# Optimization experiments

Hardware: AMD Instinct MI355X
Metric: run time of the kernel (lower is better)

## Reference

```python
import jax, jax.numpy as jnp
import numpy as np

HEADS = 16


def _rope(t):
    # t: [B, H, S, hd]. lucidrains RotaryEmbedding(dim=hd//2): rotates first hd//2
    # channels with interleaved pairs, theta=10000; remaining channels pass through.
    hd = t.shape[-1]
    rot = hd // 2
    S = t.shape[-2]
    inv_freq = 1.0 / (10000.0 ** (jnp.arange(0, rot, 2, dtype=jnp.float32) / rot))  # [rot//2]
    ang = jnp.arange(S, dtype=jnp.float32)[:, None] * inv_freq[None, :]             # [S, rot//2]
    ang = jnp.repeat(ang, 2, axis=-1)                                               # [S, rot]
    cos, sin = jnp.cos(ang), jnp.sin(ang)
    tl, tr = t[..., :rot], t[..., rot:]
    p = tl.reshape(*tl.shape[:-1], rot // 2, 2)
    rh = jnp.stack([-p[..., 1], p[..., 0]], axis=-1).reshape(tl.shape)              # rotate_half
    tl = tl * cos + rh * sin
    return jnp.concatenate([tl, tr], axis=-1)


def setup_inputs() -> dict:
    key = jax.random.key(0)
    ks = jax.random.split(key, 3)
    D = 1024
    return {
        "x": jax.random.normal(ks[0], (2, 2048, D), dtype=jnp.float32),
        "w_qkv": jax.random.normal(ks[1], (D, 3 * D), dtype=jnp.float32) * 0.02,
        "b_qkv": jnp.zeros((3 * D,), dtype=jnp.float32),
        "w_out": jax.random.normal(ks[2], (D, D), dtype=jnp.float32) * 0.02,
        "b_out": jnp.zeros((D,), dtype=jnp.float32),
        "ln_gamma": jnp.ones((D,), dtype=jnp.float32),
        "ln_beta": jnp.zeros((D,), dtype=jnp.float32),
    }


def reference(x, w_qkv, b_qkv, w_out, b_out, ln_gamma, ln_beta):
    B, S, D = x.shape
    hd = D // HEADS
    xp = x @ w_qkv + b_qkv                      # [B, S, 3D]
    q, k, v = jnp.split(xp, 3, axis=-1)
    to_heads = lambda t: t.reshape(B, S, HEADS, hd).transpose(0, 2, 1, 3)  # [B,H,S,hd]
    q, k, v = to_heads(q), to_heads(k), to_heads(v)
    q, k = _rope(q), _rope(k)
    attn = jnp.einsum('bhid,bhjd->bhij', q, k) * (D ** -0.5)  # note: scaled by full h_dim
    attn = jax.nn.softmax(attn, axis=-1)
    xv = jnp.einsum('bhij,bhjd->bhid', attn, v)
    y = xv.transpose(0, 2, 1, 3).reshape(B, S, D) + x         # residual
    y = y @ w_out + b_out
    mu = jnp.mean(y, axis=-1, keepdims=True)
    var = jnp.var(y, axis=-1, keepdims=True)
    y = (y - mu) / jnp.sqrt(var + 1e-5)
    return y * ln_gamma + ln_beta
```

## Files before the change

kernel.cpp:

```cpp
#include <hip/hip_runtime.h>
#include <hip/hip_bf16.h>
#include <math.h>

#define HEADS 16
#define HD 64
#define ROT 32
#define DM 1024
#define N3 3072
#define BB 2
#define SS 2048
#define MM 4096

typedef short short8 __attribute__((ext_vector_type(8)));
typedef float f32x4 __attribute__((ext_vector_type(4)));

__device__ __forceinline__ unsigned int pack2_bf16(float a, float b) {
    __hip_bfloat162 h = __float22bfloat162_rn(make_float2(a, b));
    unsigned int r;
    __builtin_memcpy(&r, &h, 4);
    return r;
}

__device__ __forceinline__ void gload_lds16(const void* g, void* l) {
    __builtin_amdgcn_global_load_lds(
        (const __attribute__((address_space(1))) unsigned int*)g,
        (__attribute__((address_space(3))) unsigned int*)l, 16, 0, 0);
}

__global__ __launch_bounds__(256) void conv_x(
    const float* __restrict__ x, __hip_bfloat16* __restrict__ xb)
{
    int idx = blockIdx.x * 256 + threadIdx.x;
    const float4* src = (const float4*)x;
    float4 v0 = src[idx * 2], v1 = src[idx * 2 + 1];
    uint4 o;
    o.x = pack2_bf16(v0.x, v0.y);
    o.y = pack2_bf16(v0.z, v0.w);
    o.z = pack2_bf16(v1.x, v1.y);
    o.w = pack2_bf16(v1.z, v1.w);
    ((uint4*)xb)[idx] = o;
}

__global__ __launch_bounds__(256) void tr_cast(
    const float* __restrict__ src, __hip_bfloat16* __restrict__ dst,
    int R, int C)
{
    __shared__ float t[32][33];
    const int tx = threadIdx.x, ty = threadIdx.y;
    const int c0 = blockIdx.x * 32, r0 = blockIdx.y * 32;
    #pragma unroll
    for (int k = 0; k < 4; ++k)
        t[ty + k * 8][tx] = src[(size_t)(r0 + ty + k * 8) * C + c0 + tx];
    __syncthreads();
    #pragma unroll
    for (int k = 0; k < 4; ++k)
        dst[(size_t)(c0 + ty + k * 8) * R + r0 + tx] =
            __float2bfloat16(t[tx][ty + k * 8]);
}

__global__ __launch_bounds__(256) void gemm_qkv_mfma(
    const __hip_bfloat16* __restrict__ A, const __hip_bfloat16* __restrict__ Bt,
    const float* __restrict__ bias,
    __hip_bfloat16* __restrict__ Q, __hip_bfloat16* __restrict__ K,
    __hip_bfloat16* __restrict__ Vt)
{
    __shared__ __align__(16) char Asm[8192];
    __shared__ __align__(16) char Bsm[8192];
    const int tid = threadIdx.x;
    const int wid = tid >> 6, lane = tid & 63;
    const int lg = lane >> 4, lc = lane & 15;
    const int wr = wid >> 1, wc = wid & 1;
    const int m0 = blockIdx.x * 128, n0 = blockIdx.y * 128;

    const int idx0 = wid * 128 + lane;
    const int row0 = idx0 >> 2, c16 = idx0 & 3;
    const char* Ag = (const char*)A + (size_t)(m0 + row0) * 2048 + c16 * 16;
    const char* Bg = (const char*)Bt + (size_t)(n0 + row0) * 2048 + c16 * 16;
    char* Al = Asm + wid * 2048;
    char* Bl = Bsm + wid * 2048;

    f32x4 acc[4][4];
    #pragma unroll
    for (int i = 0; i < 4; ++i)
        #pragma unroll
        for (int j = 0; j < 4; ++j) acc[i][j] = f32x4{0.f, 0.f, 0.f, 0.f};

    for (int kb = 0; kb < 2048; kb += 64) {
        if (kb) __syncthreads();
        gload_lds16(Ag + kb, Al);
        gload_lds16(Ag + 32768 + kb, Al + 1024);
        gload_lds16(Bg + kb, Bl);
        gload_lds16(Bg + 32768 + kb, Bl + 1024);
        __syncthreads();

        short8 a[4], b[4];
        #pragma unroll
        for (int mt = 0; mt < 4; ++mt)
            a[mt] = *(const short8*)(Asm + (wr * 64 + mt * 16 + lc) * 64 + lg * 16);
        #pragma unroll
        for (int nt = 0; nt < 4; ++nt)
            b[nt] = *(const short8*)(Bsm + (wc * 64 + nt * 16 + lc) * 64 + lg * 16);
        #pragma unroll
        for (int mt = 0; mt < 4; ++mt)
            #pragma unroll
            for (int nt = 0; nt < 4; ++nt)
                acc[mt][nt] = __builtin_amdgcn_mfma_f32_16x16x32_bf16(
                    a[mt], b[nt], acc[mt][nt], 0, 0, 0);
    }

    #pragma unroll
    for (int nt = 0; nt < 4; ++nt) {
        const int n = n0 + wc * 64 + nt * 16 + lc;
        const int sec = n >> 10;
        const int nd = n & 1023;
        const int h = nd >> 6, d = nd & 63;
        const float bv = bias[n];
        if (sec == 2) {
            #pragma unroll
            for (int mt = 0; mt < 4; ++mt) {
                const int mbase = m0 + wr * 64 + mt * 16 + lg * 4;
                const int s = mbase & (SS - 1);
                const int b = mbase >> 11;
                uint2 pk;
                pk.x = pack2_bf16(acc[mt][nt][0] + bv, acc[mt][nt][1] + bv);
                pk.y = pack2_bf16(acc[mt][nt][2] + bv, acc[mt][nt][3] + bv);
                *(uint2*)((char*)Vt +
                    (((size_t)(b * HEADS + h) * HD + d) * SS + s) * 2) = pk;
            }
        } else {
            const bool rope = (d < ROT);
            const float inv = exp2f(-0.8304820237f * (float)(d >> 1));
            __hip_bfloat16* dst = (sec == 0) ? Q : K;
            const float qs = (sec == 0) ? 0.04508422f : 1.0f;
            #pragma unroll
            for (int mt = 0; mt < 4; ++mt) {
                const int mbase = m0 + wr * 64 + mt * 16 + lg * 4;
                #pragma unroll
                for (int reg = 0; reg < 4; ++reg) {
                    const int m = mbase + reg;
                    const int s = m & (SS - 1);
                    const int b = m >> 11;
                    float v = acc[mt][nt][reg] + bv;
                    float partner = __shfl_xor(v, 1);
                    if (rope) {
                        float ang = (float)s * inv;
                        float cs = __cosf(ang), sn = __sinf(ang);
                        v = (lc & 1) ? (v * cs + partner * sn)
                                     : (v * cs - partner * sn);
                    }
                    v *= qs;
                    size_t o = (((size_t)(b * HEADS + h)) * SS + s) * HD + d;
                    dst[o] = __float2bfloat16(v);
                }
            }
        }
    }
}

__global__ __launch_bounds__(256) void attn_mfma(
    const __hip_bfloat16* __restrict__ Qb, const __hip_bfloat16* __restrict__ Kb,
    const __hip_bfloat16* __restrict__ Vtb, const float* __restrict__ x,
    __hip_bfloat16* __restrict__ Y1)
{
    __shared__ __align__(16) char Ksm[8192];
    __shared__ __align__(16) char Vsm[8192];
    __shared__ __align__(16) char Psm[10240];

    const int tid = threadIdx.x;
    const int wid = tid >> 6, lane = tid & 63;
    const int lg = lane >> 4, lc = lane & 15;
    const int bh = blockIdx.y;
    const int b = bh >> 4, h = bh & 15;
    const int q0 = blockIdx.x * 64;

    const int qrow = q0 + wid * 16 + lc;
    const char* qbase = (const char*)(Qb + ((size_t)bh * SS + qrow) * HD);
    short8 qf[2];
    qf[0] = *(const short8*)(qbase + lg * 16);
    qf[1] = *(const short8*)(qbase + 64 + lg * 16);

    f32x4 oacc[4];
    #pragma unroll
    for (int dt = 0; dt < 4; ++dt) oacc[dt] = f32x4{0.f, 0.f, 0.f, 0.f};
    float mrow[4]  = {-1e30f, -1e30f, -1e30f, -1e30f};
    float plsum[4] = {0.f, 0.f, 0.f, 0.f};

    const int off0 = wid * 2048 + lane * 16;
    const int off1 = off0 + 1024;
    const int r0 = off0 >> 7, blk0 = (off0 >> 4) & 7;
    const int r1 = off1 >> 7, blk1 = (off1 >> 4) & 7;
    const int sw0 = (blk0 ^ (r0 & 7)) << 4;
    const int sw1 = (blk1 ^ (r1 & 7)) << 4;
    const int ksrc0 = r0 * 128 + sw0;
    const int ksrc1 = r1 * 128 + sw1;
    const int vsrc0 = r0 * (SS * 2) + sw0;
    const int vsrc1 = r1 * (SS * 2) + sw1;
    char* ksl = Ksm + wid * 2048;
    char* vsl = Vsm + wid * 2048;
    char* Pw  = Psm + wid * 2560;

    const char* Kt  = (const char*)(Kb  + (size_t)bh * SS * HD);
    const char* Vtt = (const char*)(Vtb + (size_t)bh * SS * HD);

    for (int kt = 0; kt < SS / 64; ++kt) {
        if (kt) __syncthreads();
        const char* kg = Kt + (size_t)kt * 8192;
        const char* vg = Vtt + (size_t)kt * 128;
        gload_lds16(kg + ksrc0, ksl);
        gload_lds16(kg + ksrc1, ksl + 1024);
        gload_lds16(vg + vsrc0, vsl);
        gload_lds16(vg + vsrc1, vsl + 1024);
        __syncthreads();

        f32x4 sacc[4];
        #pragma unroll
        for (int nt = 0; nt < 4; ++nt) sacc[nt] = f32x4{0.f, 0.f, 0.f, 0.f};
        #pragma unroll
        for (int nt = 0; nt < 4; ++nt) {
            #pragma unroll
            for (int t = 0; t < 2; ++t) {
                int row = nt * 16 + lc;
                int cb = t * 64 + lg * 16;
                short8 kf = *(const short8*)(Ksm + row * 128 + (cb ^ ((row & 7) << 4)));
                sacc[nt] = __builtin_amdgcn_mfma_f32_16x16x32_bf16(qf[t], kf, sacc[nt], 0, 0, 0);
            }
        }

        float cmax[4];
        #pragma unroll
        for (int r = 0; r < 4; ++r)
            cmax[r] = fmaxf(fmaxf(sacc[0][r], sacc[1][r]),
                            fmaxf(sacc[2][r], sacc[3][r]));
        float dgrow = fmaxf(fmaxf(cmax[0] - mrow[0], cmax[1] - mrow[1]),
                            fmaxf(cmax[2] - mrow[2], cmax[3] - mrow[3]));
        if (!__all(dgrow <= 8.0f)) {
            #pragma unroll
            for (int r = 0; r < 4; ++r) {
                float mx = cmax[r];
                mx = fmaxf(mx, __shfl_xor(mx, 1));
                mx = fmaxf(mx, __shfl_xor(mx, 2));
                mx = fmaxf(mx, __shfl_xor(mx, 4));
                mx = fmaxf(mx, __shfl_xor(mx, 8));
                float mnew = fmaxf(mrow[r], mx);
                float corr = exp2f(mrow[r] - mnew);
                mrow[r] = mnew;
                plsum[r] *= corr;
                #pragma unroll
                for (int dt = 0; dt < 4; ++dt) oacc[dt][r] *= corr;
            }
        }
        #pragma unroll
        for (int nt = 0; nt < 4; ++nt) {
            float p0 = exp2f(sacc[nt][0] - mrow[0]);
            float p1 = exp2f(sacc[nt][1] - mrow[1]);
            float p2 = exp2f(sacc[nt][2] - mrow[2]);
            float p3 = exp2f(sacc[nt][3] - mrow[3]);
            plsum[0] += p0; plsum[1] += p1; plsum[2] += p2; plsum[3] += p3;
            uint2 w2;
            w2.x = pack2_bf16(p0, p1);
            w2.y = pack2_bf16(p2, p3);
            *(uint2*)(Pw + (nt * 16 + lc) * 40 + lg * 8) = w2;
        }

        short8 pf[2];
        #pragma unroll
        for (int t = 0; t < 2; ++t)
            #pragma unroll
            for (int j = 0; j < 8; ++j)
                pf[t][j] = *(const short*)(Pw + (t * 32 + lg * 8 + j) * 40 + lc * 2);
        #pragma unroll
        for (int dt = 0; dt < 4; ++dt) {
            #pragma unroll
            for (int t = 0; t < 2; ++t) {
                int vrow = dt * 16 + lc;
                int vcb = t * 64 + lg * 16;
                short8 vf = *(const short8*)(Vsm + vrow * 128 + (vcb ^ ((vrow & 7) << 4)));
                oacc[dt] = __builtin_amdgcn_mfma_f32_16x16x32_bf16(pf[t], vf, oacc[dt], 0, 0, 0);
            }
        }
    }

    #pragma unroll
    for (int r = 0; r < 4; ++r) {
        float s = plsum[r];
        s += __shfl_xor(s, 1);
        s += __shfl_xor(s, 2);
        s += __shfl_xor(s, 4);
        s += __shfl_xor(s, 8);
        float inv = 1.0f / s;
        int qr = q0 + wid * 16 + lg * 4 + r;
        size_t rowoff = ((size_t)b * SS + qr) * DM + h * HD;
        #pragma unroll
        for (int dt = 0; dt < 4; ++dt) {
            int d = dt * 16 + lc;
            Y1[rowoff + d] = __float2bfloat16(oacc[dt][r] * inv + x[rowoff + d]);
        }
    }
}

__global__ __launch_bounds__(256) void gemm_out_mfma(
    const __hip_bfloat16* __restrict__ A, const __hip_bfloat16* __restrict__ Bt,
    const float* __restrict__ bias, float* __restrict__ out)
{
    __shared__ __align__(16) char Asm[8192];
    __shared__ __align__(16) char Bsm[8192];
    const int tid = threadIdx.x;
    const int wid = tid >> 6, lane = tid & 63;
    const int lg = lane >> 4, lc = lane & 15;
    const int wr = wid >> 1, wc = wid & 1;
    const int m0 = blockIdx.x * 128, n0 = blockIdx.y * 128;

    const int idx0 = wid * 128 + lane;
    const int row0 = idx0 >> 2, c16 = idx0 & 3;
    const char* Ag = (const char*)A + (size_t)(m0 + row0) * 2048 + c16 * 16;
    const char* Bg = (const char*)Bt + (size_t)(n0 + row0) * 2048 + c16 * 16;
    char* Al = Asm + wid * 2048;
    char* Bl = Bsm + wid * 2048;

    f32x4 acc[4][4];
    #pragma unroll
    for (int i = 0; i < 4; ++i)
        #pragma unroll
        for (int j = 0; j < 4; ++j) acc[i][j] = f32x4{0.f, 0.f, 0.f, 0.f};

    for (int kb = 0; kb < 2048; kb += 64) {
        if (kb) __syncthreads();
        gload_lds16(Ag + kb, Al);
        gload_lds16(Ag + 32768 + kb, Al + 1024);
        gload_lds16(Bg + kb, Bl);
        gload_lds16(Bg + 32768 + kb, Bl + 1024);
        __syncthreads();

        short8 a[4], b[4];
        #pragma unroll
        for (int mt = 0; mt < 4; ++mt)
            a[mt] = *(const short8*)(Asm + (wr * 64 + mt * 16 + lc) * 64 + lg * 16);
        #pragma unroll
        for (int nt = 0; nt < 4; ++nt)
            b[nt] = *(const short8*)(Bsm + (wc * 64 + nt * 16 + lc) * 64 + lg * 16);
        #pragma unroll
        for (int mt = 0; mt < 4; ++mt)
            #pragma unroll
            for (int nt = 0; nt < 4; ++nt)
                acc[mt][nt] = __builtin_amdgcn_mfma_f32_16x16x32_bf16(
                    a[mt], b[nt], acc[mt][nt], 0, 0, 0);
    }

    #pragma unroll
    for (int nt = 0; nt < 4; ++nt) {
        const int n = n0 + wc * 64 + nt * 16 + lc;
        const float bv = bias[n];
        #pragma unroll
        for (int mt = 0; mt < 4; ++mt) {
            const int mbase = m0 + wr * 64 + mt * 16 + lg * 4;
            #pragma unroll
            for (int reg = 0; reg < 4; ++reg)
                out[(size_t)(mbase + reg) * DM + n] = acc[mt][nt][reg] + bv;
        }
    }
}

__global__ __launch_bounds__(256) void lnorm(
    float* __restrict__ y, const float* __restrict__ gamma,
    const float* __restrict__ beta)
{
    const int row = blockIdx.x;
    const int t = threadIdx.x;
    float* rp = y + (size_t)row * DM;
    float4 v = reinterpret_cast<float4*>(rp)[t];

    float s  = v.x + v.y + v.z + v.w;
    float ss = v.x * v.x + v.y * v.y + v.z * v.z + v.w * v.w;
    #pragma unroll
    for (int off = 32; off > 0; off >>= 1) {
        s  += __shfl_down(s, off);
        ss += __shfl_down(ss, off);
    }
    __shared__ float red[8];
    const int wid = t >> 6;
    if ((t & 63) == 0) { red[wid] = s; red[4 + wid] = ss; }
    __syncthreads();
    if (t == 0) {
        float S   = red[0] + red[1] + red[2] + red[3];
        float SSq = red[4] + red[5] + red[6] + red[7];
        float mu = S / (float)DM;
        red[0] = mu;
        red[4] = SSq / (float)DM - mu * mu;
    }
    __syncthreads();
    const float mu = red[0];
    const float rstd = rsqrtf(red[4] + 1e-5f);

    float4 g  = reinterpret_cast<const float4*>(gamma)[t];
    float4 be = reinterpret_cast<const float4*>(beta)[t];
    float4 o;
    o.x = (v.x - mu) * rstd * g.x + be.x;
    o.y = (v.y - mu) * rstd * g.y + be.y;
    o.z = (v.z - mu) * rstd * g.z + be.z;
    o.w = (v.w - mu) * rstd * g.w + be.w;
    reinterpret_cast<float4*>(rp)[t] = o;
}

extern "C" void kernel_launch(void* const* d_in, const int* in_sizes, int n_in,
                              void* d_out, int out_size, void* d_ws, size_t ws_size,
                              hipStream_t stream)
{
    const float* x      = (const float*)d_in[0];
    const float* w_qkv  = (const float*)d_in[1];
    const float* b_qkv  = (const float*)d_in[2];
    const float* w_out  = (const float*)d_in[3];
    const float* b_out  = (const float*)d_in[4];
    const float* gamma  = (const float*)d_in[5];
    const float* beta   = (const float*)d_in[6];
    float* out = (float*)d_out;
    char* wsb  = (char*)d_ws;

    __hip_bfloat16* xb  = (__hip_bfloat16*)(wsb);
    __hip_bfloat16* wqt = (__hip_bfloat16*)(wsb + (8u << 20));
    __hip_bfloat16* wot = (__hip_bfloat16*)(wsb + (14u << 20));
    __hip_bfloat16* Q   = (__hip_bfloat16*)(wsb + (16u << 20));
    __hip_bfloat16* K   = (__hip_bfloat16*)(wsb + (24u << 20));
    __hip_bfloat16* Vt  = (__hip_bfloat16*)(wsb + (32u << 20));
    __hip_bfloat16* Y1b = (__hip_bfloat16*)(wsb + (40u << 20));

    conv_x<<<2048, 256, 0, stream>>>(x, xb);
    tr_cast<<<dim3(N3 / 32, DM / 32), dim3(32, 8), 0, stream>>>(w_qkv, wqt, DM, N3);
    tr_cast<<<dim3(DM / 32, DM / 32), dim3(32, 8), 0, stream>>>(w_out, wot, DM, DM);

    dim3 g1(MM / 128, N3 / 128);
    gemm_qkv_mfma<<<g1, 256, 0, stream>>>(xb, wqt, b_qkv, Q, K, Vt);

    dim3 g2(SS / 64, BB * HEADS);
    attn_mfma<<<g2, 256, 0, stream>>>(Q, K, Vt, x, Y1b);

    dim3 g3(MM / 128, DM / 128);
    gemm_out_mfma<<<g3, 256, 0, stream>>>(Y1b, wot, b_out, out);

    lnorm<<<MM, 256, 0, stream>>>(out, gamma, beta);
}
```

Measured before the change: 237.3 us.

## Split attention key tiles across two wave groups and merge softmax partials

The attention block grows from 256 to 512 threads. Each of the four query waves gets a partner wave, and the two handle separate halves of every 64-key tile, each keeping its own online-softmax max, sum and output accumulator. The partials are merged through shared memory at the end, and K and V loads are divided between the two groups. This doubles the waves available to hide MFMA and exp latency, at the cost of extra syncs, an LDS merge step, and possible occupancy limits from the larger block.

```diff
diff --git a/kernel.cpp b/kernel.cpp
--- a/kernel.cpp
+++ b/kernel.cpp
@@ -157,23 +157,25 @@
     }
 }
 
-__global__ __launch_bounds__(256) void attn_mfma(
+__global__ __launch_bounds__(512) void attn_mfma(
     const __hip_bfloat16* __restrict__ Qb, const __hip_bfloat16* __restrict__ Kb,
     const __hip_bfloat16* __restrict__ Vtb, const float* __restrict__ x,
     __hip_bfloat16* __restrict__ Y1)
 {
-    __shared__ __align__(16) char Ksm[8192];
-    __shared__ __align__(16) char Vsm[8192];
-    __shared__ __align__(16) char Psm[10240];
+    __shared__ __align__(16) char SM[26624];
+    char* Ksm = SM;
+    char* Vsm = SM + 8192;
+    char* Psm = SM + 16384;
 
     const int tid = threadIdx.x;
     const int wid = tid >> 6, lane = tid & 63;
     const int lg = lane >> 4, lc = lane & 15;
+    const int qw = wid & 3, kh = wid >> 2;
     const int bh = blockIdx.y;
     const int b = bh >> 4, h = bh & 15;
     const int q0 = blockIdx.x * 64;
 
-    const int qrow = q0 + wid * 16 + lc;
+    const int qrow = q0 + qw * 16 + lc;
     const char* qbase = (const char*)(Qb + ((size_t)bh * SS + qrow) * HD);
     short8 qf[2];
     qf[0] = *(const short8*)(qbase + lg * 16);
@@ -185,7 +187,7 @@
     float mrow[4]  = {-1e30f, -1e30f, -1e30f, -1e30f};
     float plsum[4] = {0.f, 0.f, 0.f, 0.f};
 
-    const int off0 = wid * 2048 + lane * 16;
+    const int off0 = qw * 2048 + lane * 16;
     const int off1 = off0 + 1024;
     const int r0 = off0 >> 7, blk0 = (off0 >> 4) & 7;
     const int r1 = off1 >> 7, blk1 = (off1 >> 4) & 7;
@@ -195,31 +197,32 @@
     const int ksrc1 = r1 * 128 + sw1;
     const int vsrc0 = r0 * (SS * 2) + sw0;
     const int vsrc1 = r1 * (SS * 2) + sw1;
-    char* ksl = Ksm + wid * 2048;
-    char* vsl = Vsm + wid * 2048;
-    char* Pw  = Psm + wid * 2560;
+    char* Pw = Psm + wid * 1280;
 
     const char* Kt  = (const char*)(Kb  + (size_t)bh * SS * HD);
     const char* Vtt = (const char*)(Vtb + (size_t)bh * SS * HD);
 
     for (int kt = 0; kt < SS / 64; ++kt) {
         if (kt) __syncthreads();
-        const char* kg = Kt + (size_t)kt * 8192;
-        const char* vg = Vtt + (size_t)kt * 128;
-        gload_lds16(kg + ksrc0, ksl);
-        gload_lds16(kg + ksrc1, ksl + 1024);
-        gload_lds16(vg + vsrc0, vsl);
-        gload_lds16(vg + vsrc1, vsl + 1024);
+        if (kh == 0) {
+            const char* kg = Kt + (size_t)kt * 8192;
+            gload_lds16(kg + ksrc0, Ksm + off0);
+            gload_lds16(kg + ksrc1, Ksm + off1);
+        } else {
+            const char* vg = Vtt + (size_t)kt * 128;
+            gload_lds16(vg + vsrc0, Vsm + off0);
+            gload_lds16(vg + vsrc1, Vsm + off1);
+        }
         __syncthreads();
 
-        f32x4 sacc[4];
-        #pragma unroll
-        for (int nt = 0; nt < 4; ++nt) sacc[nt] = f32x4{0.f, 0.f, 0.f, 0.f};
-        #pragma unroll
-        for (int nt = 0; nt < 4; ++nt) {
+        f32x4 sacc[2];
+        #pragma unroll
+        for (int nt = 0; nt < 2; ++nt) sacc[nt] = f32x4{0.f, 0.f, 0.f, 0.f};
+        #pragma unroll
+        for (int nt = 0; nt < 2; ++nt) {
             #pragma unroll
             for (int t = 0; t < 2; ++t) {
-                int row = nt * 16 + lc;
+                int row = kh * 32 + nt * 16 + lc;
                 int cb = t * 64 + lg * 16;
                 short8 kf = *(const short8*)(Ksm + row * 128 + (cb ^ ((row & 7) << 4)));
                 sacc[nt] = __builtin_amdgcn_mfma_f32_16x16x32_bf16(qf[t], kf, sacc[nt], 0, 0, 0);
@@ -229,8 +232,7 @@
         float cmax[4];
         #pragma unroll
         for (int r = 0; r < 4; ++r)
-            cmax[r] = fmaxf(fmaxf(sacc[0][r], sacc[1][r]),
-                            fmaxf(sacc[2][r], sacc[3][r]));
+            cmax[r] = fmaxf(sacc[0][r], sacc[1][r]);
         float dgrow = fmaxf(fmaxf(cmax[0] - mrow[0], cmax[1] - mrow[1]),
                             fmaxf(cmax[2] - mrow[2], cmax[3] - mrow[3]));
         if (!__all(dgrow <= 8.0f)) {
@@ -250,7 +252,7 @@
             }
         }
         #pragma unroll
-        for (int nt = 0; nt < 4; ++nt) {
+        for (int nt = 0; nt < 2; ++nt) {
             float p0 = exp2f(sacc[nt][0] - mrow[0]);
             float p1 = exp2f(sacc[nt][1] - mrow[1]);
             float p2 = exp2f(sacc[nt][2] - mrow[2]);
@@ -262,38 +264,60 @@
             *(uint2*)(Pw + (nt * 16 + lc) * 40 + lg * 8) = w2;
         }
 
-        short8 pf[2];
-        #pragma unroll
-        for (int t = 0; t < 2; ++t)
-            #pragma unroll
-            for (int j = 0; j < 8; ++j)
-                pf[t][j] = *(const short*)(Pw + (t * 32 + lg * 8 + j) * 40 + lc * 2);
+        short8 pf;
+        #pragma unroll
+        for (int j = 0; j < 8; ++j)
+            pf[j] = *(const short*)(Pw + (lg * 8 + j) * 40 + lc * 2);
         #pragma unroll
         for (int dt = 0; dt < 4; ++dt) {
-            #pragma unroll
-            for (int t = 0; t < 2; ++t) {
-                int vrow = dt * 16 + lc;
-                int vcb = t * 64 + lg * 16;
-                short8 vf = *(const short8*)(Vsm + vrow * 128 + (vcb ^ ((vrow & 7) << 4)));
-                oacc[dt] = __builtin_amdgcn_mfma_f32_16x16x32_bf16(pf[t], vf, oacc[dt], 0, 0, 0);
+            int vrow = dt * 16 + lc;
+            int vcb = kh * 64 + lg * 16;
+            short8 vf = *(const short8*)(Vsm + vrow * 128 + (vcb ^ ((vrow & 7) << 4)));
+            oacc[dt] = __builtin_amdgcn_mfma_f32_16x16x32_bf16(pf, vf, oacc[dt], 0, 0, 0);
+        }
+    }
+
+    __syncthreads();
+    char* mb = SM + qw * 6144 + lane * 96;
+    if (kh == 1) {
+        #pragma unroll
+        for (int dt = 0; dt < 4; ++dt)
+            *(f32x4*)(mb + dt * 16) = oacc[dt];
+        *(f32x4*)(mb + 64) = f32x4{mrow[0], mrow[1], mrow[2], mrow[3]};
+        *(f32x4*)(mb + 80) = f32x4{plsum[0], plsum[1], plsum[2], plsum[3]};
+    }
+    __syncthreads();
+    if (kh == 0) {
+        f32x4 oB[4];
+        #pragma unroll
+        for (int dt = 0; dt < 4; ++dt) oB[dt] = *(const f32x4*)(mb + dt * 16);
+        f32x4 mB = *(const f32x4*)(mb + 64);
+        f32x4 lB = *(const f32x4*)(mb + 80);
+        #pragma unroll
+        for (int r = 0; r < 4; ++r) {
+            float m = fmaxf(mrow[r], mB[r]);
+            float wA = exp2f(mrow[r] - m);
+            float wB = exp2f(mB[r] - m);
+            plsum[r] = plsum[r] * wA + lB[r] * wB;
+            #pragma unroll
+            for (int dt = 0; dt < 4; ++dt)
+                oacc[dt][r] = oacc[dt][r] * wA + oB[dt][r] * wB;
+        }
+        #pragma unroll
+        for (int r = 0; r < 4; ++r) {
+            float s = plsum[r];
+            s += __shfl_xor(s, 1);
+            s += __shfl_xor(s, 2);
+            s += __shfl_xor(s, 4);
+            s += __shfl_xor(s, 8);
+            float inv = 1.0f / s;
+            int qr = q0 + qw * 16 + lg * 4 + r;
+            size_t rowoff = ((size_t)b * SS + qr) * DM + h * HD;
+            #pragma unroll
+            for (int dt = 0; dt < 4; ++dt) {
+                int d = dt * 16 + lc;
+                Y1[rowoff + d] = __float2bfloat16(oacc[dt][r] * inv + x[rowoff + d]);
             }
-        }
-    }
-
-    #pragma unroll
-    for (int r = 0; r < 4; ++r) {
-        float s = plsum[r];
-        s += __shfl_xor(s, 1);
-        s += __shfl_xor(s, 2);
-        s += __shfl_xor(s, 4);
-        s += __shfl_xor(s, 8);
-        float inv = 1.0f / s;
-        int qr = q0 + wid * 16 + lg * 4 + r;
-        size_t rowoff = ((size_t)b * SS + qr) * DM + h * HD;
-        #pragma unroll
-        for (int dt = 0; dt < 4; ++dt) {
-            int d = dt * 16 + lc;
-            Y1[rowoff + d] = __float2bfloat16(oacc[dt][r] * inv + x[rowoff + d]);
         }
     }
 }
@@ -431,7 +455,7 @@
     gemm_qkv_mfma<<<g1, 256, 0, stream>>>(xb, wqt, b_qkv, Q, K, Vt);
 
     dim3 g2(SS / 64, BB * HEADS);
-    attn_mfma<<<g2, 256, 0, stream>>>(Q, K, Vt, x, Y1b);
+    attn_mfma<<<g2, 512, 0, stream>>>(Q, K, Vt, x, Y1b);
 
     dim3 g3(MM / 128, DM / 128);
     gemm_out_mfma<<<g3, 256, 0, stream>>>(Y1b, wot, b_out, out);
```

Result: slower. 245.1 us (+3.3%).
